# Performance work log

Hardware: AMD Instinct MI355X
Metric: run time of the kernel (lower is better)

Reference implementation:

```python
import jax, jax.numpy as jnp
import numpy as np

B, C, L = 16, 256, 2048

def setup_inputs() -> dict:
    key = jax.random.key(0)
    y = jax.random.normal(key, (B, C, L), dtype=jnp.float32)
    alpha = jnp.float32(0.5)
    beta = jnp.float32(0.5)
    gamma = jnp.float32(0.0)
    return {"y": y, "alpha": alpha, "beta": beta, "gamma": gamma}

def reference(y, alpha, beta, gamma):
    # y: [B, C, L]
    Bs, Cs, Ls = y.shape
    # channel attention: scores over channels, scaled by 1/sqrt(L)
    scale_c = 1.0 / np.sqrt(max(Ls, 1)).astype(np.float32)
    scores_c = jnp.einsum('bcl,bdl->bcd', y, y) * scale_c          # [B, C, C]
    attn_c = jax.nn.softmax(scores_c, axis=-1)
    y_c = jnp.einsum('bcd,bdl->bcl', attn_c, y)                    # [B, C, L]
    # time attention: scores over time steps, scaled by 1/sqrt(C)
    scale_t = 1.0 / np.sqrt(max(Cs, 1)).astype(np.float32)
    scores_t = jnp.einsum('bcl,bcm->blm', y, y) * scale_t          # [B, L, L]
    attn_t = jax.nn.softmax(scores_t, axis=-1)
    y_t = jnp.einsum('blm,bcm->bcl', attn_t, y)                    # [B, C, L]
    # learnable weighted combine + residual (gamma)
    out = alpha * y_c + beta * y_t + gamma * y
    return out
```

## Files before the change

### kernel.cpp

```cpp
#include <hip/hip_runtime.h>

#define B_ 16
#define C_ 256
#define L_ 2048

typedef __attribute__((ext_vector_type(8))) short short8;
typedef __attribute__((ext_vector_type(4))) float float4v;

__device__ inline float4v mfma16(short8 a, short8 b, float4v c) {
  return __builtin_amdgcn_mfma_f32_16x16x32_bf16(a, b, c, 0, 0, 0);
}

__device__ inline ushort f2bf(float x) {
  union { float f; unsigned u; } v; v.f = x;
  unsigned r = (v.u + 0x7fffu + ((v.u >> 16) & 1u)) >> 16;
  return (ushort)r;
}

__device__ inline float bf2f(ushort u) {
  union { unsigned u; float f; } v; v.u = ((unsigned)u) << 16;
  return v.f;
}

__device__ inline void dma16(const ushort* g, void* l) {
  __builtin_amdgcn_global_load_lds(
      (const __attribute__((address_space(1))) unsigned int*)(g),
      (__attribute__((address_space(3))) unsigned int*)(l), 16, 0, 0);
}

#define BAR_VM8() asm volatile("s_waitcnt vmcnt(8)\ns_barrier" ::: "memory")
#define BAR_VM4() asm volatile("s_waitcnt vmcnt(4)\ns_barrier" ::: "memory")
#define BAR_VM0() asm volatile("s_waitcnt vmcnt(0)\ns_barrier" ::: "memory")
#define BAR_RAW() asm volatile("s_barrier" ::: "memory")
#define WAIT_VM0() asm volatile("s_waitcnt vmcnt(0)" ::: "memory")
#define WAIT_LGKM0() asm volatile("s_waitcnt lgkmcnt(0)" ::: "memory")

__global__ __launch_bounds__(256) void cvt_kernel(const float* __restrict__ y,
                                                  ushort* __restrict__ yb,
                                                  ushort* __restrict__ ytb) {
  __shared__ float tile[64][68];
  int b = blockIdx.z, ct = blockIdx.y, lt = blockIdx.x;
  int tx = threadIdx.x & 15, ty = threadIdx.x >> 4;
  size_t base = ((size_t)b * C_ + (size_t)ct * 64) * L_ + (size_t)lt * 64;
#pragma unroll
  for (int i = 0; i < 4; ++i) {
    int r = ty + i * 16;
    float4 v = *(const float4*)(y + base + (size_t)r * L_ + tx * 4);
    *(float4*)(&tile[r][tx * 4]) = v;
    ushort4 u;
    u.x = f2bf(v.x); u.y = f2bf(v.y); u.z = f2bf(v.z); u.w = f2bf(v.w);
    *(ushort4*)(yb + base + (size_t)r * L_ + tx * 4) = u;
  }
  __syncthreads();
  size_t tbase = ((size_t)b * L_ + (size_t)lt * 64) * C_ + (size_t)ct * 64;
#pragma unroll
  for (int i = 0; i < 4; ++i) {
    int r = ty + i * 16;
    ushort4 u;
    u.x = f2bf(tile[tx * 4 + 0][r]);
    u.y = f2bf(tile[tx * 4 + 1][r]);
    u.z = f2bf(tile[tx * 4 + 2][r]);
    u.w = f2bf(tile[tx * 4 + 3][r]);
    *(ushort4*)(ytb + tbase + (size_t)r * C_ + tx * 4) = u;
  }
}

__global__ __launch_bounds__(512) void pk_kernel(const ushort* __restrict__ yb,
                                                 ushort* __restrict__ Pc,
                                                 float* __restrict__ ginvC) {
  const int blk = blockIdx.x;
  const int b = (blk & 7) + 8 * ((blk >> 3) & 1);
  const int m0 = (blk >> 4) * 16;
  const int tid = threadIdx.x;
  const int w = tid >> 6, lane = tid & 63, quad = lane >> 4, l16 = lane & 15;
  const float scale = 0.022097086912079608f;
  const float SHIFT = 45.0f;

  __shared__ __align__(16) unsigned char Tb[3][32768];
  __shared__ float wsum[8][16];

  const ushort* Yb = yb + (size_t)b * C_ * L_;
  const int chq = ((lane & 3) - ((lane >> 3) & 3)) & 3;
  const int dl = (lane >> 2) * L_ + chq * 8;
  const int sK = (quad + ((l16 >> 1) & 3)) & 3;
  const int frag_lane = l16 * 64 + sK * 16;

  float4v acc[2];
#pragma unroll
  for (int nt = 0; nt < 2; ++nt) acc[nt] = (float4v){0.f, 0.f, 0.f, 0.f};

  auto PK_STAGE = [&](int t) {
    int kc = t * 64;
    unsigned char* bp = Tb[t % 3];
#pragma unroll
    for (int j = 0; j < 4; ++j) {
      int gi = w * 4 + j, kk2 = gi >> 4, chgrp = gi & 15;
      dma16(Yb + (size_t)chgrp * 16 * L_ + kc + kk2 * 32 + dl, (void*)(bp + gi * 1024));
    }
  };

  PK_STAGE(0);
  PK_STAGE(1);

  for (int c = 0; c < 32; ++c) {
    if (c == 31) { BAR_VM0(); } else { BAR_VM4(); }
    if (c < 30) PK_STAGE(c + 2);
    const unsigned char* cbuf = Tb[c % 3];
    __builtin_amdgcn_s_setprio(1);
#pragma unroll
    for (int kk2 = 0; kk2 < 2; ++kk2) {
      short8 aA = *(const short8*)(cbuf + (kk2 * 16 + (m0 >> 4)) * 1024 + frag_lane);
#pragma unroll
      for (int nt = 0; nt < 2; ++nt) {
        short8 bB = *(const short8*)(cbuf + (kk2 * 16 + w * 2 + nt) * 1024 + frag_lane);
        acc[nt] = mfma16(aA, bB, acc[nt]);
      }
    }
    __builtin_amdgcn_s_setprio(0);
  }

  float p[2][4], rs[4] = {0.f, 0.f, 0.f, 0.f};
#pragma unroll
  for (int nt = 0; nt < 2; ++nt)
#pragma unroll
    for (int r = 0; r < 4; ++r) {
      p[nt][r] = __expf(fmaf(acc[nt][r], scale, -SHIFT));
      rs[r] += p[nt][r];
    }
  ushort* Pb = Pc + ((size_t)b * 256 + m0) * 256;
#pragma unroll
  for (int nt = 0; nt < 2; ++nt)
#pragma unroll
    for (int r = 0; r < 4; ++r)
      Pb[(quad * 4 + r) * 256 + w * 32 + nt * 16 + l16] = f2bf(p[nt][r]);
#pragma unroll
  for (int r = 0; r < 4; ++r)
#pragma unroll
    for (int off = 1; off < 16; off <<= 1) rs[r] += __shfl_xor(rs[r], off);
  if (l16 == 0) {
#pragma unroll
    for (int r = 0; r < 4; ++r) wsum[w][quad * 4 + r] = rs[r];
  }
  __syncthreads();
  if (tid < 16) {
    float s = 0.f;
#pragma unroll
    for (int ww = 0; ww < 8; ++ww) s += wsum[ww][tid];
    ginvC[b * 256 + m0 + tid] = 1.0f / s;
  }
}

__global__ __launch_bounds__(256, 1) void ct_kernel(
    const ushort* __restrict__ yb, const ushort* __restrict__ ytb,
    const ushort* __restrict__ Pc, const float* __restrict__ ginvC,
    float* __restrict__ out, const float* __restrict__ alpha_p,
    const float* __restrict__ beta_p, const float* __restrict__ gamma_p) {
  const int blk = blockIdx.x;
  const int b = (blk & 7) + 8 * ((blk >> 3) & 1);
  const int m0 = (blk >> 4) * 128;
  const int tid = threadIdx.x;
  const int w = tid >> 6, lane = tid & 63, quad = lane >> 4, l16 = lane & 15;
  const float scale_t = 0.0625f;
  const float SHIFT = 16.0f;

  __shared__ __align__(16) unsigned char buf[3][32768];
  __shared__ float rsum2[2][256];

  const ushort* Yt = ytb + (size_t)b * L_ * C_;
  const ushort* Yb = yb + (size_t)b * C_ * L_;
  const ushort* Pcb = Pc + (size_t)b * 256 * 256;
  const int chq = ((lane & 3) - ((lane >> 3) & 3)) & 3;
  const int vlV = (lane >> 2) * L_ + chq * 8;
  const int pcl = (lane >> 2) * 256 + chq * 8;
  const int sK = (quad + ((l16 >> 1) & 3)) & 3;
  const int frag_lane = l16 * 64 + sK * 16;
  const int qcol0 = m0 + w * 32 + l16;
  const int qcol1 = qcol0 + 16;

  short8 Qf0[8], Qf1[8];
#pragma unroll
  for (int kk = 0; kk < 8; ++kk) {
    Qf0[kk] = *(const short8*)(Yt + (size_t)qcol0 * C_ + kk * 32 + quad * 8);
    Qf1[kk] = *(const short8*)(Yt + (size_t)qcol1 * C_ + kk * 32 + quad * 8);
  }

  const ushort* dp[8];
#pragma unroll
  for (int j = 0; j < 8; ++j) {
    int gi = w * 8 + j;
    if (gi < 16) {
      int kk = gi >> 1, g = gi & 1;
      int ridx = lane >> 2;
      int trow = g * 4 + (ridx & 3) + (ridx >> 2) * 8;
      dp[j] = Yt + (size_t)trow * C_ + kk * 32 + chq * 8;
    } else {
      int cg = gi - 16;
      dp[j] = Yb + (size_t)cg * 16 * L_ + vlV;
    }
  }
  const int dstride = (w < 2) ? 32 * C_ : 32;

  WAIT_VM0();

  float4v fc0[16], fc1[16];
#pragma unroll
  for (int ct = 0; ct < 16; ++ct) {
    fc0[ct] = (float4v){0.f, 0.f, 0.f, 0.f};
    fc1[ct] = (float4v){0.f, 0.f, 0.f, 0.f};
  }

  auto PC_STAGE = [&](int t) {
    unsigned char* bp = buf[t % 3];
#pragma unroll
    for (int j = 0; j < 4; ++j) {
      int gi = w * 4 + j;
      dma16(Pcb + (size_t)(gi * 16) * 256 + t * 32 + pcl, (void*)(bp + gi * 1024));
    }
  };

  PC_STAGE(0);
  PC_STAGE(1);

  for (int c2 = 0; c2 < 8; ++c2) {
    if (c2 == 7) { BAR_VM0(); } else { BAR_VM4(); }
    if (c2 < 6) PC_STAGE(c2 + 2);
    if (c2 == 7) {
#pragma unroll
      for (int j = 0; j < 8; ++j) {
        dma16(dp[j], (void*)(buf[0] + (w * 8 + j) * 1024));
        dp[j] += dstride;
      }
    }
    const unsigned char* cbuf = buf[c2 % 3];
    __builtin_amdgcn_s_setprio(1);
#pragma unroll
    for (int ct = 0; ct < 16; ++ct) {
      short8 Ac = *(const short8*)(cbuf + ct * 1024 + frag_lane);
      fc0[ct] = mfma16(Ac, Qf0[c2], fc0[ct]);
      fc1[ct] = mfma16(Ac, Qf1[c2], fc1[ct]);
    }
    __builtin_amdgcn_s_setprio(0);
  }
  BAR_RAW();
#pragma unroll
  for (int j = 0; j < 8; ++j) {
    dma16(dp[j], (void*)(buf[1] + (w * 8 + j) * 1024));
    dp[j] += dstride;
  }

  float4v ft0[16], ft1[16];
#pragma unroll
  for (int ct = 0; ct < 16; ++ct) {
    ft0[ct] = (float4v){0.f, 0.f, 0.f, 0.f};
    ft1[ct] = (float4v){0.f, 0.f, 0.f, 0.f};
  }
  float rs0 = 0.f, rs1 = 0.f;

  for (int c = 0; c < 64; ++c) {
    const int cb = c % 3;
    if (c == 63) { BAR_VM0(); } else { BAR_VM8(); }
    if (c < 62) {
#pragma unroll
      for (int j = 0; j < 8; ++j) {
        dma16(dp[j], (void*)(buf[(c + 2) % 3] + (w * 8 + j) * 1024));
        dp[j] += dstride;
      }
    }
    float4v s00 = (float4v){0.f, 0.f, 0.f, 0.f};
    float4v s10 = (float4v){0.f, 0.f, 0.f, 0.f};
    float4v s01 = (float4v){0.f, 0.f, 0.f, 0.f};
    float4v s11 = (float4v){0.f, 0.f, 0.f, 0.f};
    __builtin_amdgcn_s_setprio(1);
#pragma unroll
    for (int kk = 0; kk < 8; ++kk) {
      short8 k0 = *(const short8*)(buf[cb] + (kk * 2 + 0) * 1024 + frag_lane);
      short8 k1 = *(const short8*)(buf[cb] + (kk * 2 + 1) * 1024 + frag_lane);
      s00 = mfma16(k0, Qf0[kk], s00);
      s01 = mfma16(k0, Qf1[kk], s01);
      s10 = mfma16(k1, Qf0[kk], s10);
      s11 = mfma16(k1, Qf1[kk], s11);
    }
    __builtin_amdgcn_s_setprio(0);
    union PU { ushort us[8]; short8 v; } pu0, pu1;
#pragma unroll
    for (int r = 0; r < 4; ++r) {
      float a0 = __expf(fmaf(s00[r], scale_t, -SHIFT));
      float a1 = __expf(fmaf(s10[r], scale_t, -SHIFT));
      rs0 += a0 + a1;
      pu0.us[r] = f2bf(a0);
      pu0.us[4 + r] = f2bf(a1);
      float b0 = __expf(fmaf(s01[r], scale_t, -SHIFT));
      float b1 = __expf(fmaf(s11[r], scale_t, -SHIFT));
      rs1 += b0 + b1;
      pu1.us[r] = f2bf(b0);
      pu1.us[4 + r] = f2bf(b1);
    }
    short8 pb0 = pu0.v, pb1 = pu1.v;
    __builtin_amdgcn_s_setprio(1);
#pragma unroll
    for (int ct = 0; ct < 16; ++ct) {
      short8 va = *(const short8*)(buf[cb] + (16 + ct) * 1024 + frag_lane);
      ft0[ct] = mfma16(va, pb0, ft0[ct]);
      ft1[ct] = mfma16(va, pb1, ft1[ct]);
    }
    __builtin_amdgcn_s_setprio(0);
  }

  rsum2[0][tid] = rs0;
  rsum2[1][tid] = rs1;
  WAIT_LGKM0();
  float rstot0 = rsum2[0][w * 64 + l16] + rsum2[0][w * 64 + 16 + l16] +
                 rsum2[0][w * 64 + 32 + l16] + rsum2[0][w * 64 + 48 + l16];
  float rstot1 = rsum2[1][w * 64 + l16] + rsum2[1][w * 64 + 16 + l16] +
                 rsum2[1][w * 64 + 32 + l16] + rsum2[1][w * 64 + 48 + l16];

  const float alpha = alpha_p[0], beta = beta_p[0], gamma = gamma_p[0];
  const float gq0 = beta / rstot0;
  const float gq1 = beta / rstot1;

  if (gamma != 0.0f) {
#pragma unroll
    for (int ct = 0; ct < 16; ++ct) {
      float4 gcv = *(const float4*)(ginvC + b * 256 + ct * 16 + quad * 4);
#pragma unroll
      for (int r = 0; r < 4; ++r) {
        int ch = ct * 16 + quad * 4 + r;
        size_t rowb = ((size_t)b * C_ + ch) * L_;
        float g = (r == 0) ? gcv.x : (r == 1) ? gcv.y : (r == 2) ? gcv.z : gcv.w;
        float v0 = alpha * g * fc0[ct][r] + gq0 * ft0[ct][r];
        float v1 = alpha * g * fc1[ct][r] + gq1 * ft1[ct][r];
        out[rowb + qcol0] = fmaf(gamma, bf2f(Yb[(size_t)ch * L_ + qcol0]), v0);
        out[rowb + qcol1] = fmaf(gamma, bf2f(Yb[(size_t)ch * L_ + qcol1]), v1);
      }
    }
  } else {
#pragma unroll
    for (int ct = 0; ct < 16; ++ct) {
      float4 gcv = *(const float4*)(ginvC + b * 256 + ct * 16 + quad * 4);
#pragma unroll
      for (int r = 0; r < 4; ++r) {
        int ch = ct * 16 + quad * 4 + r;
        size_t rowb = ((size_t)b * C_ + ch) * L_;
        float g = (r == 0) ? gcv.x : (r == 1) ? gcv.y : (r == 2) ? gcv.z : gcv.w;
        out[rowb + qcol0] = alpha * g * fc0[ct][r] + gq0 * ft0[ct][r];
        out[rowb + qcol1] = alpha * g * fc1[ct][r] + gq1 * ft1[ct][r];
      }
    }
  }
}

extern "C" void kernel_launch(void* const* d_in, const int* in_sizes, int n_in,
                              void* d_out, int out_size, void* d_ws, size_t ws_size,
                              hipStream_t stream) {
  const float* y = (const float*)d_in[0];
  const float* alpha = (const float*)d_in[1];
  const float* beta = (const float*)d_in[2];
  const float* gamma = (const float*)d_in[3];
  float* out = (float*)d_out;

  ushort* yb = (ushort*)d_ws;
  ushort* ytb = yb + (size_t)B_ * C_ * L_;
  ushort* Pc = ytb + (size_t)B_ * C_ * L_;
  float* ginvC = (float*)(Pc + (size_t)B_ * 256 * 256);

  hipLaunchKernelGGL(cvt_kernel, dim3(L_ / 64, C_ / 64, B_), dim3(256), 0, stream,
                     y, yb, ytb);
  hipLaunchKernelGGL(pk_kernel, dim3(256), dim3(512), 0, stream, yb, Pc, ginvC);
  hipLaunchKernelGGL(ct_kernel, dim3(256), dim3(256), 0, stream,
                     yb, ytb, Pc, ginvC, out, alpha, beta, gamma);
}
```

Baseline: 250.4 us.

## Split fused kernel into channel-attention and time-attention kernels with split-K waves

Splits the fused kernel in two. The first kernel computes the channel-attention product and writes alpha-scaled partial output. The second kernel uses 512 threads in which two groups of four waves take alternating key chunks (split-K), then combine their accumulators through LDS exchange and add to the output written earlier. The aim is more waves per CU to hide latency in the time-attention loop, at the cost of an extra launch, an extra read-modify-write of the output, and the reduction exchange.

```diff
diff --git a/kernel.cpp b/kernel.cpp
--- a/kernel.cpp
+++ b/kernel.cpp
@@ -28,12 +28,9 @@
       (__attribute__((address_space(3))) unsigned int*)(l), 16, 0, 0);
 }
 
-#define BAR_VM8() asm volatile("s_waitcnt vmcnt(8)\ns_barrier" ::: "memory")
 #define BAR_VM4() asm volatile("s_waitcnt vmcnt(4)\ns_barrier" ::: "memory")
 #define BAR_VM0() asm volatile("s_waitcnt vmcnt(0)\ns_barrier" ::: "memory")
-#define BAR_RAW() asm volatile("s_barrier" ::: "memory")
 #define WAIT_VM0() asm volatile("s_waitcnt vmcnt(0)" ::: "memory")
-#define WAIT_LGKM0() asm volatile("s_waitcnt lgkmcnt(0)" ::: "memory")
 
 __global__ __launch_bounds__(256) void cvt_kernel(const float* __restrict__ y,
                                                   ushort* __restrict__ yb,
@@ -150,27 +147,21 @@
   }
 }
 
-__global__ __launch_bounds__(256, 1) void ct_kernel(
-    const ushort* __restrict__ yb, const ushort* __restrict__ ytb,
-    const ushort* __restrict__ Pc, const float* __restrict__ ginvC,
-    float* __restrict__ out, const float* __restrict__ alpha_p,
-    const float* __restrict__ beta_p, const float* __restrict__ gamma_p) {
+__global__ __launch_bounds__(256) void ck_kernel(
+    const ushort* __restrict__ ytb, const ushort* __restrict__ Pc,
+    const float* __restrict__ ginvC, float* __restrict__ out,
+    const float* __restrict__ alpha_p) {
   const int blk = blockIdx.x;
   const int b = (blk & 7) + 8 * ((blk >> 3) & 1);
   const int m0 = (blk >> 4) * 128;
   const int tid = threadIdx.x;
   const int w = tid >> 6, lane = tid & 63, quad = lane >> 4, l16 = lane & 15;
-  const float scale_t = 0.0625f;
-  const float SHIFT = 16.0f;
-
-  __shared__ __align__(16) unsigned char buf[3][32768];
-  __shared__ float rsum2[2][256];
+
+  __shared__ __align__(16) unsigned char buf[3][16384];
 
   const ushort* Yt = ytb + (size_t)b * L_ * C_;
-  const ushort* Yb = yb + (size_t)b * C_ * L_;
   const ushort* Pcb = Pc + (size_t)b * 256 * 256;
   const int chq = ((lane & 3) - ((lane >> 3) & 3)) & 3;
-  const int vlV = (lane >> 2) * L_ + chq * 8;
   const int pcl = (lane >> 2) * 256 + chq * 8;
   const int sK = (quad + ((l16 >> 1) & 3)) & 3;
   const int frag_lane = l16 * 64 + sK * 16;
@@ -183,11 +174,130 @@
     Qf0[kk] = *(const short8*)(Yt + (size_t)qcol0 * C_ + kk * 32 + quad * 8);
     Qf1[kk] = *(const short8*)(Yt + (size_t)qcol1 * C_ + kk * 32 + quad * 8);
   }
-
-  const ushort* dp[8];
-#pragma unroll
-  for (int j = 0; j < 8; ++j) {
-    int gi = w * 8 + j;
+  WAIT_VM0();
+
+  float4v fc0[16], fc1[16];
+#pragma unroll
+  for (int ct = 0; ct < 16; ++ct) {
+    fc0[ct] = (float4v){0.f, 0.f, 0.f, 0.f};
+    fc1[ct] = (float4v){0.f, 0.f, 0.f, 0.f};
+  }
+
+  auto PC_STAGE = [&](int t) {
+    unsigned char* bp = buf[t % 3];
+#pragma unroll
+    for (int j = 0; j < 4; ++j) {
+      int gi = w * 4 + j;
+      dma16(Pcb + (size_t)(gi * 16) * 256 + t * 32 + pcl, (void*)(bp + gi * 1024));
+    }
+  };
+
+  PC_STAGE(0);
+  PC_STAGE(1);
+
+#pragma unroll
+  for (int c2 = 0; c2 < 8; ++c2) {
+    if (c2 == 7) { BAR_VM0(); } else { BAR_VM4(); }
+    if (c2 < 6) PC_STAGE(c2 + 2);
+    const unsigned char* cbuf = buf[c2 % 3];
+    __builtin_amdgcn_s_setprio(1);
+#pragma unroll
+    for (int ct = 0; ct < 16; ++ct) {
+      short8 Ac = *(const short8*)(cbuf + ct * 1024 + frag_lane);
+      fc0[ct] = mfma16(Ac, Qf0[c2], fc0[ct]);
+      fc1[ct] = mfma16(Ac, Qf1[c2], fc1[ct]);
+    }
+    __builtin_amdgcn_s_setprio(0);
+  }
+
+  const float alpha = alpha_p[0];
+#pragma unroll
+  for (int ct = 0; ct < 16; ++ct) {
+    float4 gcv = *(const float4*)(ginvC + b * 256 + ct * 16 + quad * 4);
+#pragma unroll
+    for (int r = 0; r < 4; ++r) {
+      int ch = ct * 16 + quad * 4 + r;
+      size_t rowb = ((size_t)b * C_ + ch) * L_;
+      float g = (r == 0) ? gcv.x : (r == 1) ? gcv.y : (r == 2) ? gcv.z : gcv.w;
+      out[rowb + qcol0] = alpha * g * fc0[ct][r];
+      out[rowb + qcol1] = alpha * g * fc1[ct][r];
+    }
+  }
+}
+
+#define XCHG_WRITE(CTB)                                                    \
+  _Pragma("unroll") for (int i = 0; i < 4; ++i) {                          \
+    float4 t0, t1;                                                         \
+    t0.x = ft0[(CTB) + i][0]; t0.y = ft0[(CTB) + i][1];                    \
+    t0.z = ft0[(CTB) + i][2]; t0.w = ft0[(CTB) + i][3];                    \
+    t1.x = ft1[(CTB) + i][0]; t1.y = ft1[(CTB) + i][1];                    \
+    t1.z = ft1[(CTB) + i][2]; t1.w = ft1[(CTB) + i][3];                    \
+    xb[(i * 2 + 0) * 64 + lane] = t0;                                      \
+    xb[(i * 2 + 1) * 64 + lane] = t1;                                      \
+  }
+
+#define XCHG_ADD(CTB)                                                      \
+  _Pragma("unroll") for (int i = 0; i < 4; ++i) {                          \
+    float4 t0 = xbp[(i * 2 + 0) * 64 + lane];                              \
+    float4 t1 = xbp[(i * 2 + 1) * 64 + lane];                              \
+    ft0[(CTB) + i][0] += t0.x; ft0[(CTB) + i][1] += t0.y;                  \
+    ft0[(CTB) + i][2] += t0.z; ft0[(CTB) + i][3] += t0.w;                  \
+    ft1[(CTB) + i][0] += t1.x; ft1[(CTB) + i][1] += t1.y;                  \
+    ft1[(CTB) + i][2] += t1.z; ft1[(CTB) + i][3] += t1.w;                  \
+  }
+
+#define TT_EPI(CTB, DO_GAMMA)                                              \
+  _Pragma("unroll") for (int c8 = 0; c8 < 8; ++c8) {                       \
+    _Pragma("unroll") for (int r = 0; r < 4; ++r) {                        \
+      int ch = ((CTB) + c8) * 16 + quad * 4 + r;                           \
+      size_t rowb = ((size_t)b * C_ + ch) * L_;                            \
+      float v0 = out[rowb + qcol0] + gq0 * ft0[(CTB) + c8][r];             \
+      float v1 = out[rowb + qcol1] + gq1 * ft1[(CTB) + c8][r];             \
+      if (DO_GAMMA) {                                                      \
+        v0 = fmaf(gamma, bf2f(Yb[(size_t)ch * L_ + qcol0]), v0);           \
+        v1 = fmaf(gamma, bf2f(Yb[(size_t)ch * L_ + qcol1]), v1);           \
+      }                                                                    \
+      out[rowb + qcol0] = v0;                                              \
+      out[rowb + qcol1] = v1;                                              \
+    }                                                                      \
+  }
+
+__global__ __launch_bounds__(512, 2) void tt_kernel(
+    const ushort* __restrict__ yb, const ushort* __restrict__ ytb,
+    float* __restrict__ out, const float* __restrict__ beta_p,
+    const float* __restrict__ gamma_p) {
+  const int blk = blockIdx.x;
+  const int b = (blk & 7) + 8 * ((blk >> 3) & 1);
+  const int m0 = (blk >> 4) * 128;
+  const int tid = threadIdx.x;
+  const int w = tid >> 6, lane = tid & 63, quad = lane >> 4, l16 = lane & 15;
+  const int qw = w & 3, tpar = w >> 2;
+  const float scale_t = 0.0625f;
+  const float SHIFT = 16.0f;
+
+  __shared__ __align__(16) unsigned char buf[3][32768];
+  __shared__ float rsum[2][2][256];
+
+  const ushort* Yt = ytb + (size_t)b * L_ * C_;
+  const ushort* Yb = yb + (size_t)b * C_ * L_;
+  const int chq = ((lane & 3) - ((lane >> 3) & 3)) & 3;
+  const int vlV = (lane >> 2) * L_ + chq * 8;
+  const int sK = (quad + ((l16 >> 1) & 3)) & 3;
+  const int frag_lane = l16 * 64 + sK * 16;
+  const int qcol0 = m0 + qw * 32 + l16;
+  const int qcol1 = qcol0 + 16;
+
+  short8 Qf0[8], Qf1[8];
+#pragma unroll
+  for (int kk = 0; kk < 8; ++kk) {
+    Qf0[kk] = *(const short8*)(Yt + (size_t)qcol0 * C_ + kk * 32 + quad * 8);
+    Qf1[kk] = *(const short8*)(Yt + (size_t)qcol1 * C_ + kk * 32 + quad * 8);
+  }
+
+  const ushort* dp[4];
+#pragma unroll
+  for (int j = 0; j < 4; ++j) {
+    int gi = w * 4 + j;
     if (gi < 16) {
       int kk = gi >> 1, g = gi & 1;
       int ridx = lane >> 2;
@@ -198,55 +308,21 @@
       dp[j] = Yb + (size_t)cg * 16 * L_ + vlV;
     }
   }
-  const int dstride = (w < 2) ? 32 * C_ : 32;
+  const int dstride = (w < 4) ? 32 * C_ : 32;
 
   WAIT_VM0();
 
-  float4v fc0[16], fc1[16];
-#pragma unroll
-  for (int ct = 0; ct < 16; ++ct) {
-    fc0[ct] = (float4v){0.f, 0.f, 0.f, 0.f};
-    fc1[ct] = (float4v){0.f, 0.f, 0.f, 0.f};
-  }
-
-  auto PC_STAGE = [&](int t) {
+  auto TSTAGE = [&](int t) {
     unsigned char* bp = buf[t % 3];
 #pragma unroll
     for (int j = 0; j < 4; ++j) {
-      int gi = w * 4 + j;
-      dma16(Pcb + (size_t)(gi * 16) * 256 + t * 32 + pcl, (void*)(bp + gi * 1024));
+      dma16(dp[j], (void*)(bp + (w * 4 + j) * 1024));
+      dp[j] += dstride;
     }
   };
 
-  PC_STAGE(0);
-  PC_STAGE(1);
-
-  for (int c2 = 0; c2 < 8; ++c2) {
-    if (c2 == 7) { BAR_VM0(); } else { BAR_VM4(); }
-    if (c2 < 6) PC_STAGE(c2 + 2);
-    if (c2 == 7) {
-#pragma unroll
-      for (int j = 0; j < 8; ++j) {
-        dma16(dp[j], (void*)(buf[0] + (w * 8 + j) * 1024));
-        dp[j] += dstride;
-      }
-    }
-    const unsigned char* cbuf = buf[c2 % 3];
-    __builtin_amdgcn_s_setprio(1);
-#pragma unroll
-    for (int ct = 0; ct < 16; ++ct) {
-      short8 Ac = *(const short8*)(cbuf + ct * 1024 + frag_lane);
-      fc0[ct] = mfma16(Ac, Qf0[c2], fc0[ct]);
-      fc1[ct] = mfma16(Ac, Qf1[c2], fc1[ct]);
-    }
-    __builtin_amdgcn_s_setprio(0);
-  }
-  BAR_RAW();
-#pragma unroll
-  for (int j = 0; j < 8; ++j) {
-    dma16(dp[j], (void*)(buf[1] + (w * 8 + j) * 1024));
-    dp[j] += dstride;
-  }
+  TSTAGE(0);
+  TSTAGE(1);
 
   float4v ft0[16], ft1[16];
 #pragma unroll
@@ -257,95 +333,82 @@
   float rs0 = 0.f, rs1 = 0.f;
 
   for (int c = 0; c < 64; ++c) {
-    const int cb = c % 3;
-    if (c == 63) { BAR_VM0(); } else { BAR_VM8(); }
-    if (c < 62) {
-#pragma unroll
-      for (int j = 0; j < 8; ++j) {
-        dma16(dp[j], (void*)(buf[(c + 2) % 3] + (w * 8 + j) * 1024));
-        dp[j] += dstride;
+    if (c == 63) { BAR_VM0(); } else { BAR_VM4(); }
+    if (c < 62) TSTAGE(c + 2);
+    if ((c & 1) == tpar) {
+      const unsigned char* cbuf = buf[c % 3];
+      float4v s00 = (float4v){0.f, 0.f, 0.f, 0.f};
+      float4v s10 = (float4v){0.f, 0.f, 0.f, 0.f};
+      float4v s01 = (float4v){0.f, 0.f, 0.f, 0.f};
+      float4v s11 = (float4v){0.f, 0.f, 0.f, 0.f};
+      __builtin_amdgcn_s_setprio(1);
+#pragma unroll
+      for (int kk = 0; kk < 8; ++kk) {
+        short8 k0 = *(const short8*)(cbuf + (kk * 2 + 0) * 1024 + frag_lane);
+        short8 k1 = *(const short8*)(cbuf + (kk * 2 + 1) * 1024 + frag_lane);
+        s00 = mfma16(k0, Qf0[kk], s00);
+        s01 = mfma16(k0, Qf1[kk], s01);
+        s10 = mfma16(k1, Qf0[kk], s10);
+        s11 = mfma16(k1, Qf1[kk], s11);
       }
-    }
-    float4v s00 = (float4v){0.f, 0.f, 0.f, 0.f};
-    float4v s10 = (float4v){0.f, 0.f, 0.f, 0.f};
-    float4v s01 = (float4v){0.f, 0.f, 0.f, 0.f};
-    float4v s11 = (float4v){0.f, 0.f, 0.f, 0.f};
-    __builtin_amdgcn_s_setprio(1);
-#pragma unroll
-    for (int kk = 0; kk < 8; ++kk) {
-      short8 k0 = *(const short8*)(buf[cb] + (kk * 2 + 0) * 1024 + frag_lane);
-      short8 k1 = *(const short8*)(buf[cb] + (kk * 2 + 1) * 1024 + frag_lane);
-      s00 = mfma16(k0, Qf0[kk], s00);
-      s01 = mfma16(k0, Qf1[kk], s01);
-      s10 = mfma16(k1, Qf0[kk], s10);
-      s11 = mfma16(k1, Qf1[kk], s11);
-    }
-    __builtin_amdgcn_s_setprio(0);
-    union PU { ushort us[8]; short8 v; } pu0, pu1;
-#pragma unroll
-    for (int r = 0; r < 4; ++r) {
-      float a0 = __expf(fmaf(s00[r], scale_t, -SHIFT));
-      float a1 = __expf(fmaf(s10[r], scale_t, -SHIFT));
-      rs0 += a0 + a1;
-      pu0.us[r] = f2bf(a0);
-      pu0.us[4 + r] = f2bf(a1);
-      float b0 = __expf(fmaf(s01[r], scale_t, -SHIFT));
-      float b1 = __expf(fmaf(s11[r], scale_t, -SHIFT));
-      rs1 += b0 + b1;
-      pu1.us[r] = f2bf(b0);
-      pu1.us[4 + r] = f2bf(b1);
-    }
-    short8 pb0 = pu0.v, pb1 = pu1.v;
-    __builtin_amdgcn_s_setprio(1);
-#pragma unroll
-    for (int ct = 0; ct < 16; ++ct) {
-      short8 va = *(const short8*)(buf[cb] + (16 + ct) * 1024 + frag_lane);
-      ft0[ct] = mfma16(va, pb0, ft0[ct]);
-      ft1[ct] = mfma16(va, pb1, ft1[ct]);
-    }
-    __builtin_amdgcn_s_setprio(0);
-  }
-
-  rsum2[0][tid] = rs0;
-  rsum2[1][tid] = rs1;
-  WAIT_LGKM0();
-  float rstot0 = rsum2[0][w * 64 + l16] + rsum2[0][w * 64 + 16 + l16] +
-                 rsum2[0][w * 64 + 32 + l16] + rsum2[0][w * 64 + 48 + l16];
-  float rstot1 = rsum2[1][w * 64 + l16] + rsum2[1][w * 64 + 16 + l16] +
-                 rsum2[1][w * 64 + 32 + l16] + rsum2[1][w * 64 + 48 + l16];
-
-  const float alpha = alpha_p[0], beta = beta_p[0], gamma = gamma_p[0];
+      __builtin_amdgcn_s_setprio(0);
+      union PU { ushort us[8]; short8 v; } pu0, pu1;
+#pragma unroll
+      for (int r = 0; r < 4; ++r) {
+        float a0 = __expf(fmaf(s00[r], scale_t, -SHIFT));
+        float a1 = __expf(fmaf(s10[r], scale_t, -SHIFT));
+        rs0 += a0 + a1;
+        pu0.us[r] = f2bf(a0);
+        pu0.us[4 + r] = f2bf(a1);
+        float b0 = __expf(fmaf(s01[r], scale_t, -SHIFT));
+        float b1 = __expf(fmaf(s11[r], scale_t, -SHIFT));
+        rs1 += b0 + b1;
+        pu1.us[r] = f2bf(b0);
+        pu1.us[4 + r] = f2bf(b1);
+      }
+      short8 pb0 = pu0.v, pb1 = pu1.v;
+      __builtin_amdgcn_s_setprio(1);
+#pragma unroll
+      for (int ct = 0; ct < 16; ++ct) {
+        short8 va = *(const short8*)(cbuf + (16 + ct) * 1024 + frag_lane);
+        ft0[ct] = mfma16(va, pb0, ft0[ct]);
+        ft1[ct] = mfma16(va, pb1, ft1[ct]);
+      }
+      __builtin_amdgcn_s_setprio(0);
+    }
+  }
+
+  rsum[tpar][0][qw * 64 + lane] = rs0;
+  rsum[tpar][1][qw * 64 + lane] = rs1;
+
+  float4* xb = (float4*)(&buf[0][0]) + w * 512;
+  float4* xbp = (float4*)(&buf[0][0]) + (w ^ 4) * 512;
+  __syncthreads();
+  if (tpar == 0) { XCHG_WRITE(8) } else { XCHG_WRITE(0) }
+  __syncthreads();
+  if (tpar == 0) { XCHG_ADD(0) } else { XCHG_ADD(8) }
+  __syncthreads();
+  if (tpar == 0) { XCHG_WRITE(12) } else { XCHG_WRITE(4) }
+  __syncthreads();
+  if (tpar == 0) { XCHG_ADD(4) } else { XCHG_ADD(12) }
+
+  float rstot0 = 0.f, rstot1 = 0.f;
+#pragma unroll
+  for (int tp = 0; tp < 2; ++tp)
+#pragma unroll
+    for (int qd = 0; qd < 4; ++qd) {
+      rstot0 += rsum[tp][0][qw * 64 + qd * 16 + l16];
+      rstot1 += rsum[tp][1][qw * 64 + qd * 16 + l16];
+    }
+
+  const float beta = beta_p[0], gamma = gamma_p[0];
   const float gq0 = beta / rstot0;
   const float gq1 = beta / rstot1;
 
   if (gamma != 0.0f) {
-#pragma unroll
-    for (int ct = 0; ct < 16; ++ct) {
-      float4 gcv = *(const float4*)(ginvC + b * 256 + ct * 16 + quad * 4);
-#pragma unroll
-      for (int r = 0; r < 4; ++r) {
-        int ch = ct * 16 + quad * 4 + r;
-        size_t rowb = ((size_t)b * C_ + ch) * L_;
-        float g = (r == 0) ? gcv.x : (r == 1) ? gcv.y : (r == 2) ? gcv.z : gcv.w;
-        float v0 = alpha * g * fc0[ct][r] + gq0 * ft0[ct][r];
-        float v1 = alpha * g * fc1[ct][r] + gq1 * ft1[ct][r];
-        out[rowb + qcol0] = fmaf(gamma, bf2f(Yb[(size_t)ch * L_ + qcol0]), v0);
-        out[rowb + qcol1] = fmaf(gamma, bf2f(Yb[(size_t)ch * L_ + qcol1]), v1);
-      }
-    }
+    if (tpar == 0) { TT_EPI(0, 1) } else { TT_EPI(8, 1) }
   } else {
-#pragma unroll
-    for (int ct = 0; ct < 16; ++ct) {
-      float4 gcv = *(const float4*)(ginvC + b * 256 + ct * 16 + quad * 4);
-#pragma unroll
-      for (int r = 0; r < 4; ++r) {
-        int ch = ct * 16 + quad * 4 + r;
-        size_t rowb = ((size_t)b * C_ + ch) * L_;
-        float g = (r == 0) ? gcv.x : (r == 1) ? gcv.y : (r == 2) ? gcv.z : gcv.w;
-        out[rowb + qcol0] = alpha * g * fc0[ct][r] + gq0 * ft0[ct][r];
-        out[rowb + qcol1] = alpha * g * fc1[ct][r] + gq1 * ft1[ct][r];
-      }
-    }
+    if (tpar == 0) { TT_EPI(0, 0) } else { TT_EPI(8, 0) }
   }
 }
 
@@ -366,6 +429,8 @@
   hipLaunchKernelGGL(cvt_kernel, dim3(L_ / 64, C_ / 64, B_), dim3(256), 0, stream,
                      y, yb, ytb);
   hipLaunchKernelGGL(pk_kernel, dim3(256), dim3(512), 0, stream, yb, Pc, ginvC);
-  hipLaunchKernelGGL(ct_kernel, dim3(256), dim3(256), 0, stream,
-                     yb, ytb, Pc, ginvC, out, alpha, beta, gamma);
-}
+  hipLaunchKernelGGL(ck_kernel, dim3(256), dim3(256), 0, stream,
+                     ytb, Pc, ginvC, out, alpha);
+  hipLaunchKernelGGL(tt_kernel, dim3(256), dim3(512), 0, stream,
+                     yb, ytb, out, beta, gamma);
+}
```

After: 238.0 us. 4.9% less time.

## Split time-attention blocks over channel halves for two blocks per CU

Applied to the files above, without the earlier changes.

The fused time-attention kernel now gives each block 64 query columns instead of 128 and launches twice as many blocks. Within a block the four waves form two query subgroups times two channel halves, so each wave keeps half the output accumulators. LDS staging drops from triple to double buffering, with a full vmcnt(0) wait every iteration, so two blocks can fit per CU. The aim is more waves in flight to hide latency. The cost is that each query subgroup's score MFMAs and exp work are now done twice (once per channel half), K/V tiles are streamed twice as often overall, and prefetch depth is shallower.

```diff
diff --git a/kernel.cpp b/kernel.cpp
--- a/kernel.cpp
+++ b/kernel.cpp
@@ -28,10 +28,8 @@
       (__attribute__((address_space(3))) unsigned int*)(l), 16, 0, 0);
 }
 
-#define BAR_VM8() asm volatile("s_waitcnt vmcnt(8)\ns_barrier" ::: "memory")
 #define BAR_VM4() asm volatile("s_waitcnt vmcnt(4)\ns_barrier" ::: "memory")
 #define BAR_VM0() asm volatile("s_waitcnt vmcnt(0)\ns_barrier" ::: "memory")
-#define BAR_RAW() asm volatile("s_barrier" ::: "memory")
 #define WAIT_VM0() asm volatile("s_waitcnt vmcnt(0)" ::: "memory")
 #define WAIT_LGKM0() asm volatile("s_waitcnt lgkmcnt(0)" ::: "memory")
 
@@ -150,20 +148,21 @@
   }
 }
 
-__global__ __launch_bounds__(256, 1) void ct_kernel(
+__global__ __launch_bounds__(256, 2) void ct_kernel(
     const ushort* __restrict__ yb, const ushort* __restrict__ ytb,
     const ushort* __restrict__ Pc, const float* __restrict__ ginvC,
     float* __restrict__ out, const float* __restrict__ alpha_p,
     const float* __restrict__ beta_p, const float* __restrict__ gamma_p) {
   const int blk = blockIdx.x;
   const int b = (blk & 7) + 8 * ((blk >> 3) & 1);
-  const int m0 = (blk >> 4) * 128;
+  const int m0 = (blk >> 4) * 64;
   const int tid = threadIdx.x;
   const int w = tid >> 6, lane = tid & 63, quad = lane >> 4, l16 = lane & 15;
+  const int qsg = w & 1, chh = w >> 1;
   const float scale_t = 0.0625f;
   const float SHIFT = 16.0f;
 
-  __shared__ __align__(16) unsigned char buf[3][32768];
+  __shared__ __align__(16) unsigned char buf[2][32768];
   __shared__ float rsum2[2][256];
 
   const ushort* Yt = ytb + (size_t)b * L_ * C_;
@@ -174,7 +173,7 @@
   const int pcl = (lane >> 2) * 256 + chq * 8;
   const int sK = (quad + ((l16 >> 1) & 3)) & 3;
   const int frag_lane = l16 * 64 + sK * 16;
-  const int qcol0 = m0 + w * 32 + l16;
+  const int qcol0 = m0 + qsg * 32 + l16;
   const int qcol1 = qcol0 + 16;
 
   short8 Qf0[8], Qf1[8];
@@ -202,15 +201,15 @@
 
   WAIT_VM0();
 
-  float4v fc0[16], fc1[16];
-#pragma unroll
-  for (int ct = 0; ct < 16; ++ct) {
+  float4v fc0[8], fc1[8];
+#pragma unroll
+  for (int ct = 0; ct < 8; ++ct) {
     fc0[ct] = (float4v){0.f, 0.f, 0.f, 0.f};
     fc1[ct] = (float4v){0.f, 0.f, 0.f, 0.f};
   }
 
   auto PC_STAGE = [&](int t) {
-    unsigned char* bp = buf[t % 3];
+    unsigned char* bp = buf[t & 1];
 #pragma unroll
     for (int j = 0; j < 4; ++j) {
       int gi = w * 4 + j;
@@ -219,53 +218,49 @@
   };
 
   PC_STAGE(0);
-  PC_STAGE(1);
 
   for (int c2 = 0; c2 < 8; ++c2) {
-    if (c2 == 7) { BAR_VM0(); } else { BAR_VM4(); }
-    if (c2 < 6) PC_STAGE(c2 + 2);
-    if (c2 == 7) {
+    const int cb = c2 & 1;
+    BAR_VM0();
+    if (c2 < 7) {
+      PC_STAGE(c2 + 1);
+    } else {
 #pragma unroll
       for (int j = 0; j < 8; ++j) {
         dma16(dp[j], (void*)(buf[0] + (w * 8 + j) * 1024));
         dp[j] += dstride;
       }
     }
-    const unsigned char* cbuf = buf[c2 % 3];
+    const unsigned char* cbuf = buf[cb];
     __builtin_amdgcn_s_setprio(1);
 #pragma unroll
-    for (int ct = 0; ct < 16; ++ct) {
-      short8 Ac = *(const short8*)(cbuf + ct * 1024 + frag_lane);
+    for (int ct = 0; ct < 8; ++ct) {
+      short8 Ac = *(const short8*)(cbuf + (chh * 8 + ct) * 1024 + frag_lane);
       fc0[ct] = mfma16(Ac, Qf0[c2], fc0[ct]);
       fc1[ct] = mfma16(Ac, Qf1[c2], fc1[ct]);
     }
     __builtin_amdgcn_s_setprio(0);
   }
-  BAR_RAW();
-#pragma unroll
-  for (int j = 0; j < 8; ++j) {
-    dma16(dp[j], (void*)(buf[1] + (w * 8 + j) * 1024));
-    dp[j] += dstride;
-  }
-
-  float4v ft0[16], ft1[16];
-#pragma unroll
-  for (int ct = 0; ct < 16; ++ct) {
+
+  float4v ft0[8], ft1[8];
+#pragma unroll
+  for (int ct = 0; ct < 8; ++ct) {
     ft0[ct] = (float4v){0.f, 0.f, 0.f, 0.f};
     ft1[ct] = (float4v){0.f, 0.f, 0.f, 0.f};
   }
   float rs0 = 0.f, rs1 = 0.f;
 
   for (int c = 0; c < 64; ++c) {
-    const int cb = c % 3;
-    if (c == 63) { BAR_VM0(); } else { BAR_VM8(); }
-    if (c < 62) {
+    const int cb = c & 1;
+    BAR_VM0();
+    if (c < 63) {
 #pragma unroll
       for (int j = 0; j < 8; ++j) {
-        dma16(dp[j], (void*)(buf[(c + 2) % 3] + (w * 8 + j) * 1024));
+        dma16(dp[j], (void*)(buf[cb ^ 1] + (w * 8 + j) * 1024));
         dp[j] += dstride;
       }
     }
+    const unsigned char* cbuf = buf[cb];
     float4v s00 = (float4v){0.f, 0.f, 0.f, 0.f};
     float4v s10 = (float4v){0.f, 0.f, 0.f, 0.f};
     float4v s01 = (float4v){0.f, 0.f, 0.f, 0.f};
@@ -273,8 +268,8 @@
     __builtin_amdgcn_s_setprio(1);
 #pragma unroll
     for (int kk = 0; kk < 8; ++kk) {
-      short8 k0 = *(const short8*)(buf[cb] + (kk * 2 + 0) * 1024 + frag_lane);
-      short8 k1 = *(const short8*)(buf[cb] + (kk * 2 + 1) * 1024 + frag_lane);
+      short8 k0 = *(const short8*)(cbuf + (kk * 2 + 0) * 1024 + frag_lane);
+      short8 k1 = *(const short8*)(cbuf + (kk * 2 + 1) * 1024 + frag_lane);
       s00 = mfma16(k0, Qf0[kk], s00);
       s01 = mfma16(k0, Qf1[kk], s01);
       s10 = mfma16(k1, Qf0[kk], s10);
@@ -298,8 +293,8 @@
     short8 pb0 = pu0.v, pb1 = pu1.v;
     __builtin_amdgcn_s_setprio(1);
 #pragma unroll
-    for (int ct = 0; ct < 16; ++ct) {
-      short8 va = *(const short8*)(buf[cb] + (16 + ct) * 1024 + frag_lane);
+    for (int ct = 0; ct < 8; ++ct) {
+      short8 va = *(const short8*)(cbuf + (16 + chh * 8 + ct) * 1024 + frag_lane);
       ft0[ct] = mfma16(va, pb0, ft0[ct]);
       ft1[ct] = mfma16(va, pb1, ft1[ct]);
     }
@@ -320,11 +315,12 @@
 
   if (gamma != 0.0f) {
 #pragma unroll
-    for (int ct = 0; ct < 16; ++ct) {
-      float4 gcv = *(const float4*)(ginvC + b * 256 + ct * 16 + quad * 4);
+    for (int ct = 0; ct < 8; ++ct) {
+      int cglob = chh * 8 + ct;
+      float4 gcv = *(const float4*)(ginvC + b * 256 + cglob * 16 + quad * 4);
 #pragma unroll
       for (int r = 0; r < 4; ++r) {
-        int ch = ct * 16 + quad * 4 + r;
+        int ch = cglob * 16 + quad * 4 + r;
         size_t rowb = ((size_t)b * C_ + ch) * L_;
         float g = (r == 0) ? gcv.x : (r == 1) ? gcv.y : (r == 2) ? gcv.z : gcv.w;
         float v0 = alpha * g * fc0[ct][r] + gq0 * ft0[ct][r];
@@ -335,11 +331,12 @@
     }
   } else {
 #pragma unroll
-    for (int ct = 0; ct < 16; ++ct) {
-      float4 gcv = *(const float4*)(ginvC + b * 256 + ct * 16 + quad * 4);
+    for (int ct = 0; ct < 8; ++ct) {
+      int cglob = chh * 8 + ct;
+      float4 gcv = *(const float4*)(ginvC + b * 256 + cglob * 16 + quad * 4);
 #pragma unroll
       for (int r = 0; r < 4; ++r) {
-        int ch = ct * 16 + quad * 4 + r;
+        int ch = cglob * 16 + quad * 4 + r;
         size_t rowb = ((size_t)b * C_ + ch) * L_;
         float g = (r == 0) ? gcv.x : (r == 1) ? gcv.y : (r == 2) ? gcv.z : gcv.w;
         out[rowb + qcol0] = alpha * g * fc0[ct][r] + gq0 * ft0[ct][r];
@@ -366,6 +363,6 @@
   hipLaunchKernelGGL(cvt_kernel, dim3(L_ / 64, C_ / 64, B_), dim3(256), 0, stream,
                      y, yb, ytb);
   hipLaunchKernelGGL(pk_kernel, dim3(256), dim3(512), 0, stream, yb, Pc, ginvC);
-  hipLaunchKernelGGL(ct_kernel, dim3(256), dim3(256), 0, stream,
+  hipLaunchKernelGGL(ct_kernel, dim3(512), dim3(256), 0, stream,
                      yb, ytb, Pc, ginvC, out, alpha, beta, gamma);
 }
```

Measured after the change: 225.4 us. 1.11x faster.
